# Performance work log

Hardware: AMD Instinct MI355X
Metric: run time of the kernel (lower is better)

The kernel has to match this reference:

```python
import jax, jax.numpy as jnp
import numpy as np

N, E, H, Q, M, B, L = 100000, 800000, 64, 4, 8, 100, 4
EPS_BN = 1e-5


def setup_inputs() -> dict:
    key = jax.random.key(0)
    ki = iter(jax.random.split(key, 32))
    def nrm(shape, scale=1.0):
        return jax.random.normal(next(ki), shape, dtype=jnp.float32) * scale
    inp = {}
    inp["x"] = nrm((N, H))
    inp["pe"] = nrm((N, Q, M, 2))
    inp["Lam"] = jax.random.uniform(next(ki), (B, Q, M), jnp.float32, 0.0, 2.0)
    inp["edge_attr"] = nrm((E, H))
    # per-layer eigenvalue MLP phi: scalar -> 16 -> scalar
    inp["phi_w1"] = nrm((L, 1, 16))
    inp["phi_b1"] = jnp.zeros((L, 16), jnp.float32)
    inp["phi_w2"] = nrm((L, 16, 1), 0.25)
    inp["phi_b2"] = jnp.zeros((L, 1), jnp.float32)
    # per-layer edge PE encoder linear: [2*Q*M -> H]
    inp["enc_w"] = nrm((L, 2 * Q * M, H), (2.0 / (2 * Q * M)) ** 0.5)
    inp["enc_b"] = jnp.zeros((L, H), jnp.float32)
    # per-layer GINE edge linear
    inp["lin_w"] = nrm((L, H, H), (2.0 / H) ** 0.5)
    inp["lin_b"] = jnp.zeros((L, H), jnp.float32)
    # per-layer GINE MLP: Linear -> BN -> ReLU -> Linear
    inp["mlp_w1"] = nrm((L, H, H), (2.0 / H) ** 0.5)
    inp["mlp_b1"] = jnp.zeros((L, H), jnp.float32)
    inp["bn1_g"] = jnp.ones((L, H), jnp.float32)
    inp["bn1_b"] = jnp.zeros((L, H), jnp.float32)
    inp["mlp_w2"] = nrm((L, H, H), (2.0 / H) ** 0.5)
    inp["mlp_b2"] = jnp.zeros((L, H), jnp.float32)
    # per-layer outer BatchNorm
    inp["bn2_g"] = jnp.ones((L, H), jnp.float32)
    inp["bn2_b"] = jnp.zeros((L, H), jnp.float32)
    inp["edge_index"] = jax.random.randint(next(ki), (2, E), 0, N, dtype=jnp.int32)
    inp["batch"] = jnp.sort(jax.random.randint(next(ki), (N,), 0, B, dtype=jnp.int32))
    return inp


def _bn(h, g, b):
    # training-mode BatchNorm1d over the node/row axis
    mu = h.mean(axis=0)
    var = h.var(axis=0)
    return (h - mu) * jax.lax.rsqrt(var + EPS_BN) * g + b


def _forward(x, pe, Lam, edge_attr, params, edge_index, batch):
    (phi_w1, phi_b1, phi_w2, phi_b2, enc_w, enc_b, lin_w, lin_b,
     mlp_w1, mlp_b1, bn1_g, bn1_b, mlp_w2, mlp_b2, bn2_g, bn2_b) = params
    src, dst = edge_index[0], edge_index[1]
    # permutation-invariant complex edge features: pe[src] * conj(pe[dst]), per (q, eigvec)
    zs_re, zs_im = pe[src, ..., 0], pe[src, ..., 1]   # [E, Q, M]
    zd_re, zd_im = pe[dst, ..., 0], pe[dst, ..., 1]
    z_re = zs_re * zd_re + zs_im * zd_im              # [E, Q, M]
    z_im = zs_im * zd_re - zs_re * zd_im
    eg = batch[src]                                    # graph id per edge  [E]
    for l in range(L):
        # eigenvalue MLP -> per-eigenvector weight  [B, Q, M]
        hphi = jax.nn.relu(Lam[..., None] @ phi_w1[l] + phi_b1[l])   # [B,Q,M,16]
        w = (hphi @ phi_w2[l])[..., 0] + phi_b2[l][0]                # [B,Q,M]
        we = w[eg]                                                   # [E,Q,M]
        feat = jnp.concatenate([(z_re * we).reshape(E, Q * M),
                                (z_im * we).reshape(E, Q * M)], axis=-1)  # [E, 2QM]
        edge_pe = feat @ enc_w[l] + enc_b[l]                          # [E,H]
        ea = edge_pe + edge_attr
        # GINE message: ReLU(x_j + lin(edge_attr)), sum-aggregated at dst
        msg = jax.nn.relu(x[src] + ea @ lin_w[l] + lin_b[l])          # [E,H]
        agg = jax.ops.segment_sum(msg, dst, num_segments=N)           # [N,H]
        h = x + agg                                                   # (1+eps)*x with eps=0
        h = jax.nn.relu(_bn(h @ mlp_w1[l] + mlp_b1[l], bn1_g[l], bn1_b[l]))
        h = h @ mlp_w2[l] + mlp_b2[l]
        x = _bn(h, bn2_g[l], bn2_b[l])
        if l != L - 1:
            x = jax.nn.relu(x)
    return x


def reference(x, pe, Lam, edge_attr, phi_w1, phi_b1, phi_w2, phi_b2, enc_w, enc_b,
              lin_w, lin_b, mlp_w1, mlp_b1, bn1_g, bn1_b, mlp_w2, mlp_b2, bn2_g, bn2_b,
              edge_index, batch):
    params = (phi_w1, phi_b1, phi_w2, phi_b2, enc_w, enc_b, lin_w, lin_b,
              mlp_w1, mlp_b1, bn1_g, bn1_b, mlp_w2, mlp_b2, bn2_g, bn2_b)
    return (_forward(x, pe, Lam, edge_attr, params, edge_index, batch), pe)
```

## Files before the change

### kernel.cpp

```cpp
#include <hip/hip_runtime.h>

#define N_NODES 100000
#define N_EDGES 800000
#define HD 64
#define NB 100
#define NL 4
#define QM 32
#define EPS_BN 1e-5f

typedef __bf16 bf16_t;
typedef __bf16 bf16x8 __attribute__((ext_vector_type(8)));
typedef float f32x4 __attribute__((ext_vector_type(4)));


__global__ void k_count(const int* __restrict__ dst, int* __restrict__ counts) {
    int e = blockIdx.x * 256 + threadIdx.x;
    if (e < N_EDGES) atomicAdd(&counts[dst[e]], 1);
}

__global__ void k_scan1(const int* __restrict__ counts, int* __restrict__ row_ptr,
                        int* __restrict__ blk) {
    __shared__ int s[1024];
    int i = blockIdx.x * 1024 + threadIdx.x;
    int v = (i < N_NODES) ? counts[i] : 0;
    s[threadIdx.x] = v;
    __syncthreads();
    for (int off = 1; off < 1024; off <<= 1) {
        int u = (threadIdx.x >= off) ? s[threadIdx.x - off] : 0;
        __syncthreads();
        s[threadIdx.x] += u;
        __syncthreads();
    }
    if (i < N_NODES) row_ptr[i] = s[threadIdx.x] - v;
    if (threadIdx.x == 1023) blk[blockIdx.x] = s[1023];
}

__global__ void k_scan2(int* __restrict__ blk) {
    __shared__ int s[128];
    int t = threadIdx.x;
    int v = (t < 98) ? blk[t] : 0;
    s[t] = v;
    __syncthreads();
    for (int off = 1; off < 128; off <<= 1) {
        int u = (t >= off) ? s[t - off] : 0;
        __syncthreads();
        s[t] += u;
        __syncthreads();
    }
    if (t < 98) blk[t] = s[t] - v;
}

__global__ void k_scan3(const int* __restrict__ blk, int* __restrict__ row_ptr) {
    int i = blockIdx.x * 1024 + threadIdx.x;
    if (i < N_NODES) row_ptr[i] += blk[blockIdx.x];
    if (i == 0) row_ptr[N_NODES] = N_EDGES;
}

__global__ void k_scatter(const int* __restrict__ ei, const int* __restrict__ batch,
                          const int* __restrict__ row_ptr, int* __restrict__ counts,
                          int* __restrict__ src_s, int* __restrict__ eg_s,
                          int* __restrict__ dst_s, int* __restrict__ pos_of) {
    int e = blockIdx.x * 256 + threadIdx.x;
    if (e >= N_EDGES) return;
    int s = ei[e], d = ei[N_EDGES + e];
    int pos = row_ptr[d] + atomicAdd(&counts[d], 1);
    pos_of[e] = pos;
    src_s[pos] = s;
    eg_s[pos]  = batch[s];
    dst_s[pos] = d;
}

__global__ void k_permute(const float* __restrict__ pe, const float* __restrict__ edge_attr,
                          const int* __restrict__ ei, const int* __restrict__ pos_of,
                          bf16_t* __restrict__ z_s, bf16_t* __restrict__ ea_s) {
    int t = blockIdx.x * 256 + threadIdx.x;
    int e = t >> 3, j = t & 7;
    if (e >= N_EDGES) return;
    int pos = pos_of[e];
    {
        const float* ap = edge_attr + (size_t)e * 64 + j * 8;
        f32x4 a0 = *(const f32x4*)ap, a1 = *(const f32x4*)(ap + 4);
        bf16x8 o;
#pragma unroll
        for (int i = 0; i < 4; i++) { o[i] = (bf16_t)a0[i]; o[i + 4] = (bf16_t)a1[i]; }
        *(bf16x8*)(ea_s + (size_t)pos * 64 + j * 8) = o;
    }
    int s = ei[e], d = ei[N_EDGES + e];
    int jq = j & 3;
    const float* ps = pe + (size_t)s * 64 + jq * 16;
    const float* pd = pe + (size_t)d * 64 + jq * 16;
    f32x4 s0 = *(const f32x4*)ps, s1 = *(const f32x4*)(ps + 4);
    f32x4 s2 = *(const f32x4*)(ps + 8), s3 = *(const f32x4*)(ps + 12);
    f32x4 d0 = *(const f32x4*)pd, d1 = *(const f32x4*)(pd + 4);
    f32x4 d2 = *(const f32x4*)(pd + 8), d3 = *(const f32x4*)(pd + 12);
    float sv[16], dv[16];
#pragma unroll
    for (int i = 0; i < 4; i++) {
        sv[i] = s0[i]; sv[4 + i] = s1[i]; sv[8 + i] = s2[i]; sv[12 + i] = s3[i];
        dv[i] = d0[i]; dv[4 + i] = d1[i]; dv[8 + i] = d2[i]; dv[12 + i] = d3[i];
    }
    bool isim = (j >= 4);
    bf16x8 o;
#pragma unroll
    for (int i = 0; i < 8; i++) {
        float sr = sv[2 * i], si = sv[2 * i + 1];
        float dr = dv[2 * i], di = dv[2 * i + 1];
        float v = isim ? (si * dr - sr * di) : (sr * dr + si * di);
        o[i] = (bf16_t)v;
    }
    *(bf16x8*)(z_s + (size_t)pos * 64 + j * 8) = o;
}


__global__ void k_phi(const float* __restrict__ Lam, const float* __restrict__ w1,
                      const float* __restrict__ b1, const float* __restrict__ w2,
                      const float* __restrict__ b2, bf16_t* __restrict__ w_all) {
    int idx = blockIdx.x * 256 + threadIdx.x;
    if (idx >= NL * NB * QM) return;
    int l = idx / (NB * QM);
    int rem = idx % (NB * QM);
    float lam = Lam[rem];
    float acc = b2[l];
    for (int i = 0; i < 16; i++) {
        float h = lam * w1[l * 16 + i] + b1[l * 16 + i];
        acc += fmaxf(h, 0.f) * w2[l * 16 + i];
    }
    w_all[idx] = (bf16_t)acc;
}

__global__ void k_prep(const float* __restrict__ enc_w, const float* __restrict__ enc_b,
                       const float* __restrict__ lin_w, const float* __restrict__ lin_b,
                       const float* __restrict__ mlp_w1, const float* __restrict__ mlp_w2,
                       bf16_t* __restrict__ wcat_frag, bf16_t* __restrict__ w1frag,
                       bf16_t* __restrict__ w2frag, float* __restrict__ cvec) {
    __shared__ float lds[128][64];
    int l = blockIdx.x, tid = threadIdx.x;
    const float* ew = enc_w + l * 64 * 64;
    const float* lw = lin_w + l * 64 * 64;
    for (int idx = tid; idx < 64 * 64; idx += 256) {
        int r = idx >> 6, c = idx & 63;
        float acc = 0.f;
        for (int k = 0; k < 64; k++) acc += ew[r * 64 + k] * lw[k * 64 + c];
        lds[r][c] = acc;
        lds[64 + r][c] = lw[r * 64 + c];
    }
    if (tid < 64) {
        float acc = lin_b[l * 64 + tid];
        for (int k = 0; k < 64; k++) acc += enc_b[l * 64 + k] * lw[k * 64 + tid];
        cvec[l * 64 + tid] = acc;
    }
    __syncthreads();
    for (int idx = tid; idx < 16 * 512; idx += 256) {
        int sn = idx >> 9, lane = (idx >> 3) & 63, j = idx & 7;
        int s = sn >> 2, nt = sn & 3;
        int row = 32 * s + (lane >> 4) * 8 + j;
        int col = 16 * nt + (lane & 15);
        wcat_frag[l * 8192 + idx] = (bf16_t)lds[row][col];
    }
    for (int idx = tid; idx < 8 * 512; idx += 256) {
        int sn = idx >> 9, lane = (idx >> 3) & 63, j = idx & 7;
        int s = sn >> 2, nt = sn & 3;
        int row = 32 * s + (lane >> 4) * 8 + j;
        int col = 16 * nt + (lane & 15);
        w1frag[l * 4096 + idx] = (bf16_t)mlp_w1[(l * 64 + row) * 64 + col];
        w2frag[l * 4096 + idx] = (bf16_t)mlp_w2[(l * 64 + row) * 64 + col];
    }
}


__global__ void k_hinit(const float* __restrict__ x, float* __restrict__ h) {
    size_t i = ((size_t)blockIdx.x * 256 + threadIdx.x) * 8;
    if (i >= (size_t)N_NODES * 64) return;
    *(f32x4*)(h + i) = *(const f32x4*)(x + i);
    *(f32x4*)(h + i + 4) = *(const f32x4*)(x + i + 4);
}

__global__ void k_edge(const bf16_t* __restrict__ z_s, const bf16_t* __restrict__ ea_s,
                       const int* __restrict__ src_s, const int* __restrict__ eg_s,
                       const int* __restrict__ dst_s, const int* __restrict__ row_ptr,
                       const bf16_t* __restrict__ w_l, const bf16_t* __restrict__ wcat_l,
                       const float* __restrict__ cvec_l, const float* __restrict__ x_cur,
                       float* __restrict__ h) {
    __shared__ float msg[128][68];
    int tid = threadIdx.x;
    int wave = tid >> 6, lane = tid & 63;
    int quad = lane >> 4, l16 = lane & 15;
    int e0 = blockIdx.x * 128;

    bf16x8 bfrag[4][4];
    const bf16x8* wf = (const bf16x8*)wcat_l;
#pragma unroll
    for (int s = 0; s < 4; s++)
#pragma unroll
        for (int nt = 0; nt < 4; nt++) bfrag[s][nt] = wf[(s * 4 + nt) * 64 + lane];

    f32x4 acc[2][4];
#pragma unroll
    for (int rt = 0; rt < 2; rt++)
#pragma unroll
        for (int nt = 0; nt < 4; nt++) acc[rt][nt] = (f32x4)(0.f);

    int em[2];
    bf16x8 wch[2];
#pragma unroll
    for (int rt = 0; rt < 2; rt++) {
        em[rt] = e0 + wave * 32 + rt * 16 + l16;
        int eg = eg_s[em[rt]];
        wch[rt] = *(const bf16x8*)(w_l + (size_t)eg * QM + quad * 8);
    }
#pragma unroll
    for (int s = 0; s < 4; s++) {
        bf16x8 afr[2];
#pragma unroll
        for (int rt = 0; rt < 2; rt++) {
            if (s < 2) {
                bf16x8 z = *(const bf16x8*)(z_s + (size_t)em[rt] * 64 + s * 32 + quad * 8);
                bf16x8 a;
#pragma unroll
                for (int i = 0; i < 8; i++) a[i] = (bf16_t)((float)z[i] * (float)wch[rt][i]);
                afr[rt] = a;
            } else {
                afr[rt] = *(const bf16x8*)(ea_s + (size_t)em[rt] * 64 + (s - 2) * 32 + quad * 8);
            }
        }
#pragma unroll
        for (int rt = 0; rt < 2; rt++)
#pragma unroll
            for (int nt = 0; nt < 4; nt++)
                acc[rt][nt] = __builtin_amdgcn_mfma_f32_16x16x32_bf16(afr[rt], bfrag[s][nt],
                                                                     acc[rt][nt], 0, 0, 0);
    }
#pragma unroll
    for (int nt = 0; nt < 4; nt++) {
        float cv = cvec_l[nt * 16 + l16];
#pragma unroll
        for (int rt = 0; rt < 2; rt++)
#pragma unroll
            for (int r = 0; r < 4; r++)
                msg[wave * 32 + rt * 16 + quad * 4 + r][nt * 16 + l16] = acc[rt][nt][r] + cv;
    }
    __syncthreads();
    {
        int j = tid >> 1, half = tid & 1;
        int srcn = src_s[e0 + j];
        const float* xp = x_cur + (size_t)srcn * 64 + half * 32;
        float* mrow = &msg[j][half * 32];
#pragma unroll
        for (int g = 0; g < 8; g++) {
            f32x4 xv = *(const f32x4*)(xp + g * 4);
            f32x4 m = *(const f32x4*)(mrow + g * 4);
#pragma unroll
            for (int k = 0; k < 4; k++) m[k] = fmaxf(m[k] + xv[k], 0.f);
            *(f32x4*)(mrow + g * 4) = m;
        }
    }
    __syncthreads();
    int nfirst = dst_s[e0], nlast = dst_s[e0 + 127];
    int c = tid & 63;
    for (int n = nfirst + (tid >> 6); n <= nlast; n += 4) {
        int rs = row_ptr[n], re = row_ptr[n + 1];
        int a = rs > e0 ? rs : e0;
        int b = re < e0 + 128 ? re : e0 + 128;
        if (a >= b) continue;
        float sum = 0.f;
        for (int jj = a; jj < b; jj++) sum += msg[jj - e0][c];
        float* addr = h + (size_t)n * 64 + c;
        if (rs >= e0 && re <= e0 + 128) *addr += sum;
        else atomicAdd(addr, sum);
    }
}

__global__ void k_mlp1(const float* __restrict__ h, const bf16_t* __restrict__ w1frag_l,
                       const float* __restrict__ b1_l, bf16_t* __restrict__ t,
                       float* __restrict__ stats) {
    __shared__ float sred[128];
    int tid = threadIdx.x, wave = tid >> 6, lane = tid & 63, quad = lane >> 4, l16 = lane & 15;
    int r0 = blockIdx.x * 128;
    bf16x8 bfrag[2][4];
    const bf16x8* wf = (const bf16x8*)w1frag_l;
#pragma unroll
    for (int s = 0; s < 2; s++)
#pragma unroll
        for (int nt = 0; nt < 4; nt++) bfrag[s][nt] = wf[(s * 4 + nt) * 64 + lane];
    f32x4 acc[2][4];
#pragma unroll
    for (int rt = 0; rt < 2; rt++)
#pragma unroll
        for (int nt = 0; nt < 4; nt++) acc[rt][nt] = (f32x4)(0.f);
#pragma unroll
    for (int rt = 0; rt < 2; rt++) {
        int n = r0 + wave * 32 + rt * 16 + l16;
        bool valid = n < N_NODES;
#pragma unroll
        for (int s = 0; s < 2; s++) {
            bf16x8 a;
            if (valid) {
                const float* hp = h + (size_t)n * 64 + s * 32 + quad * 8;
                f32x4 v0 = *(const f32x4*)hp, v1 = *(const f32x4*)(hp + 4);
#pragma unroll
                for (int i = 0; i < 4; i++) { a[i] = (bf16_t)v0[i]; a[i + 4] = (bf16_t)v1[i]; }
            } else {
#pragma unroll
                for (int i = 0; i < 8; i++) a[i] = (bf16_t)0.f;
            }
#pragma unroll
            for (int nt = 0; nt < 4; nt++)
                acc[rt][nt] = __builtin_amdgcn_mfma_f32_16x16x32_bf16(a, bfrag[s][nt],
                                                                     acc[rt][nt], 0, 0, 0);
        }
    }
    if (tid < 128) sred[tid] = 0.f;
    __syncthreads();
#pragma unroll
    for (int nt = 0; nt < 4; nt++) {
        int col = nt * 16 + l16;
        float bias = b1_l[col];
        float s1 = 0.f, s2 = 0.f;
#pragma unroll
        for (int rt = 0; rt < 2; rt++)
#pragma unroll
            for (int r = 0; r < 4; r++) {
                int n = r0 + wave * 32 + rt * 16 + quad * 4 + r;
                if (n < N_NODES) {
                    float v = acc[rt][nt][r] + bias;
                    t[(size_t)n * 64 + col] = (bf16_t)v;
                    s1 += v; s2 += v * v;
                }
            }
        s1 += __shfl_xor(s1, 16); s1 += __shfl_xor(s1, 32);
        s2 += __shfl_xor(s2, 16); s2 += __shfl_xor(s2, 32);
        if (quad == 0) { atomicAdd(&sred[col], s1); atomicAdd(&sred[64 + col], s2); }
    }
    __syncthreads();
    if (tid < 128) atomicAdd(&stats[tid], sred[tid]);
}

__global__ void k_bncoef(const float* __restrict__ stats, const float* __restrict__ g,
                         const float* __restrict__ b, float* __restrict__ coef) {
    int c = threadIdx.x;
    if (c >= 64) return;
    float mean = stats[c] / (float)N_NODES;
    float var = stats[64 + c] / (float)N_NODES - mean * mean;
    float a = g[c] * rsqrtf(var + EPS_BN);
    coef[c] = a;
    coef[64 + c] = b[c] - mean * a;
}

__global__ void k_mlp2(const bf16_t* __restrict__ t, const float* __restrict__ coef,
                       const bf16_t* __restrict__ w2frag_l, const float* __restrict__ b2_l,
                       float* __restrict__ h2, float* __restrict__ stats2) {
    __shared__ float sred[128];
    int tid = threadIdx.x, wave = tid >> 6, lane = tid & 63, quad = lane >> 4, l16 = lane & 15;
    int r0 = blockIdx.x * 128;
    bf16x8 bfrag[2][4];
    const bf16x8* wf = (const bf16x8*)w2frag_l;
#pragma unroll
    for (int s = 0; s < 2; s++)
#pragma unroll
        for (int nt = 0; nt < 4; nt++) bfrag[s][nt] = wf[(s * 4 + nt) * 64 + lane];
    f32x4 acc[2][4];
#pragma unroll
    for (int rt = 0; rt < 2; rt++)
#pragma unroll
        for (int nt = 0; nt < 4; nt++) acc[rt][nt] = (f32x4)(0.f);
#pragma unroll
    for (int rt = 0; rt < 2; rt++) {
        int n = r0 + wave * 32 + rt * 16 + l16;
        bool valid = n < N_NODES;
#pragma unroll
        for (int s = 0; s < 2; s++) {
            bf16x8 a;
            if (valid) {
                bf16x8 tv = *(const bf16x8*)(t + (size_t)n * 64 + s * 32 + quad * 8);
                int kb = s * 32 + quad * 8;
#pragma unroll
                for (int i = 0; i < 8; i++) {
                    float y = (float)tv[i] * coef[kb + i] + coef[64 + kb + i];
                    a[i] = (bf16_t)fmaxf(y, 0.f);
                }
            } else {
#pragma unroll
                for (int i = 0; i < 8; i++) a[i] = (bf16_t)0.f;
            }
#pragma unroll
            for (int nt = 0; nt < 4; nt++)
                acc[rt][nt] = __builtin_amdgcn_mfma_f32_16x16x32_bf16(a, bfrag[s][nt],
                                                                     acc[rt][nt], 0, 0, 0);
        }
    }
    if (tid < 128) sred[tid] = 0.f;
    __syncthreads();
#pragma unroll
    for (int nt = 0; nt < 4; nt++) {
        int col = nt * 16 + l16;
        float bias = b2_l[col];
        float s1 = 0.f, s2 = 0.f;
#pragma unroll
        for (int rt = 0; rt < 2; rt++)
#pragma unroll
            for (int r = 0; r < 4; r++) {
                int n = r0 + wave * 32 + rt * 16 + quad * 4 + r;
                if (n < N_NODES) {
                    float v = acc[rt][nt][r] + bias;
                    h2[(size_t)n * 64 + col] = v;
                    s1 += v; s2 += v * v;
                }
            }
        s1 += __shfl_xor(s1, 16); s1 += __shfl_xor(s1, 32);
        s2 += __shfl_xor(s2, 16); s2 += __shfl_xor(s2, 32);
        if (quad == 0) { atomicAdd(&sred[col], s1); atomicAdd(&sred[64 + col], s2); }
    }
    __syncthreads();
    if (tid < 128) atomicAdd(&stats2[tid], sred[tid]);
}

__global__ void k_bnapply(const float* __restrict__ h2, const float* __restrict__ coef,
                          float* __restrict__ out, int do_relu) {
    size_t i = ((size_t)blockIdx.x * 256 + threadIdx.x) * 8;
    if (i >= (size_t)N_NODES * 64) return;
    int c0 = (int)(i & 63);
    f32x4 a = *(const f32x4*)(h2 + i), b = *(const f32x4*)(h2 + i + 4);
    f32x4 oa, ob;
#pragma unroll
    for (int k = 0; k < 4; k++) {
        float y0 = a[k] * coef[c0 + k] + coef[64 + c0 + k];
        float y1 = b[k] * coef[c0 + 4 + k] + coef[64 + c0 + 4 + k];
        if (do_relu) { y0 = fmaxf(y0, 0.f); y1 = fmaxf(y1, 0.f); }
        oa[k] = y0; ob[k] = y1;
    }
    *(f32x4*)(out + i) = oa;
    *(f32x4*)(out + i + 4) = ob;
}


extern "C" void kernel_launch(void* const* d_in, const int* in_sizes, int n_in,
                              void* d_out, int out_size, void* d_ws, size_t ws_size,
                              hipStream_t stream) {
    const float* x_in   = (const float*)d_in[0];
    const float* pe     = (const float*)d_in[1];
    const float* Lam    = (const float*)d_in[2];
    const float* eattr  = (const float*)d_in[3];
    const float* phi_w1 = (const float*)d_in[4];
    const float* phi_b1 = (const float*)d_in[5];
    const float* phi_w2 = (const float*)d_in[6];
    const float* phi_b2 = (const float*)d_in[7];
    const float* enc_w  = (const float*)d_in[8];
    const float* enc_b  = (const float*)d_in[9];
    const float* lin_w  = (const float*)d_in[10];
    const float* lin_b  = (const float*)d_in[11];
    const float* mlp_w1 = (const float*)d_in[12];
    const float* mlp_b1 = (const float*)d_in[13];
    const float* bn1_g  = (const float*)d_in[14];
    const float* bn1_b  = (const float*)d_in[15];
    const float* mlp_w2 = (const float*)d_in[16];
    const float* mlp_b2 = (const float*)d_in[17];
    const float* bn2_g  = (const float*)d_in[18];
    const float* bn2_b  = (const float*)d_in[19];
    const int* edge_index = (const int*)d_in[20];
    const int* batch      = (const int*)d_in[21];
    float* out = (float*)d_out;

    char* ws = (char*)d_ws;
    size_t off = 0;
    auto alloc = [&](size_t bytes) -> void* {
        void* p = ws + off;
        off += (bytes + 255) & ~(size_t)255;
        return p;
    };
    bf16_t* z_s       = (bf16_t*)alloc((size_t)N_EDGES * 64 * 2);
    bf16_t* ea_s      = (bf16_t*)alloc((size_t)N_EDGES * 64 * 2);
    int* src_s        = (int*)alloc((size_t)N_EDGES * 4);
    int* eg_s         = (int*)alloc((size_t)N_EDGES * 4);
    int* dst_s        = (int*)alloc((size_t)N_EDGES * 4);
    int* pos_of       = (int*)alloc((size_t)N_EDGES * 4);
    int* counts       = (int*)alloc((size_t)N_NODES * 4);
    int* row_ptr      = (int*)alloc((size_t)(N_NODES + 1) * 4);
    int* blk          = (int*)alloc(128 * 4);
    float* h          = (float*)alloc((size_t)N_NODES * 64 * 4);
    bf16_t* t         = (bf16_t*)alloc((size_t)N_NODES * 64 * 2);
    float* h2         = (float*)alloc((size_t)N_NODES * 64 * 4);
    float* x_cur      = (float*)alloc((size_t)N_NODES * 64 * 4);
    bf16_t* w_all     = (bf16_t*)alloc((size_t)NL * NB * QM * 2);
    bf16_t* wcat_frag = (bf16_t*)alloc((size_t)NL * 8192 * 2);
    bf16_t* w1frag    = (bf16_t*)alloc((size_t)NL * 4096 * 2);
    bf16_t* w2frag    = (bf16_t*)alloc((size_t)NL * 4096 * 2);
    float* cvec       = (float*)alloc((size_t)NL * 64 * 4);
    float* stats      = (float*)alloc(256 * 4);
    float* bncoef     = (float*)alloc(256 * 4);

    hipMemsetAsync(counts, 0, (size_t)N_NODES * 4, stream);
    k_count<<<3125, 256, 0, stream>>>(edge_index + N_EDGES, counts);
    k_scan1<<<98, 1024, 0, stream>>>(counts, row_ptr, blk);
    k_scan2<<<1, 128, 0, stream>>>(blk);
    k_scan3<<<98, 1024, 0, stream>>>(blk, row_ptr);
    hipMemsetAsync(counts, 0, (size_t)N_NODES * 4, stream);
    k_scatter<<<3125, 256, 0, stream>>>(edge_index, batch, row_ptr, counts,
                                        src_s, eg_s, dst_s, pos_of);
    k_permute<<<25000, 256, 0, stream>>>(pe, eattr, edge_index, pos_of, z_s, ea_s);
    k_phi<<<50, 256, 0, stream>>>(Lam, phi_w1, phi_b1, phi_w2, phi_b2, w_all);
    k_prep<<<NL, 256, 0, stream>>>(enc_w, enc_b, lin_w, lin_b, mlp_w1, mlp_w2,
                                   wcat_frag, w1frag, w2frag, cvec);

    for (int l = 0; l < NL; l++) {
        const float* xp = (l == 0) ? x_in : x_cur;
        hipMemsetAsync(stats, 0, 256 * 4, stream);
        k_hinit<<<3125, 256, 0, stream>>>(xp, h);
        k_edge<<<6250, 256, 0, stream>>>(z_s, ea_s, src_s, eg_s, dst_s, row_ptr,
                                         w_all + (size_t)l * NB * QM,
                                         wcat_frag + (size_t)l * 8192,
                                         cvec + (size_t)l * 64, xp, h);
        k_mlp1<<<782, 256, 0, stream>>>(h, w1frag + (size_t)l * 4096,
                                        mlp_b1 + l * 64, t, stats);
        k_bncoef<<<1, 64, 0, stream>>>(stats, bn1_g + l * 64, bn1_b + l * 64, bncoef);
        k_mlp2<<<782, 256, 0, stream>>>(t, bncoef, w2frag + (size_t)l * 4096,
                                        mlp_b2 + l * 64, h2, stats + 128);
        k_bncoef<<<1, 64, 0, stream>>>(stats + 128, bn2_g + l * 64, bn2_b + l * 64,
                                       bncoef + 128);
        float* outp = (l < NL - 1) ? x_cur : out;
        k_bnapply<<<3125, 256, 0, stream>>>(h2, bncoef + 128, outp, (l < NL - 1) ? 1 : 0);
    }
    hipMemcpyAsync(out + (size_t)N_NODES * 64, pe, (size_t)N_NODES * QM * 2 * 4,
                   hipMemcpyDeviceToDevice, stream);
}
```

Baseline: 1.312 ms.

## Pack edge metadata, interleave features, fuse BN coef and h-init into neighbours

Packs per-edge src/dst/graph/orig-id into one int4 array and interleaves z and edge_attr into a single 128-wide bf16 feature row per sorted edge. The permute kernel reads through the sorted index instead of scattering writes. The BN coefficient kernels are folded into mlp2 and the apply kernels. The apply kernel also writes the next layer's h init and a bf16 copy of x, which removes the separate hinit pass and makes the edge kernel's x[src] gather read bf16. The trade-off is extra rounding of node features to bf16, plus redundant per-block recomputation of the BN coefficients.

After: 1.194 ms. -9.0%, faster.

```diff
diff --git a/kernel.cpp b/kernel.cpp
--- a/kernel.cpp
+++ b/kernel.cpp
@@ -2,7 +2,6 @@
 
 #define N_NODES 100000
 #define N_EDGES 800000
-#define HD 64
 #define NB 100
 #define NL 4
 #define QM 32
@@ -10,6 +9,8 @@
 
 typedef __bf16 bf16_t;
 typedef __bf16 bf16x8 __attribute__((ext_vector_type(8)));
+typedef __bf16 bf16x4 __attribute__((ext_vector_type(4)));
+typedef __bf16 bf16x2 __attribute__((ext_vector_type(2)));
 typedef float f32x4 __attribute__((ext_vector_type(4)));
 
 
@@ -57,58 +58,35 @@
 }
 
 __global__ void k_scatter(const int* __restrict__ ei, const int* __restrict__ batch,
-                          const int* __restrict__ row_ptr, int* __restrict__ counts,
-                          int* __restrict__ src_s, int* __restrict__ eg_s,
-                          int* __restrict__ dst_s, int* __restrict__ pos_of) {
+                          const int* __restrict__ row_ptr, int* __restrict__ cursor,
+                          int4* __restrict__ edat) {
     int e = blockIdx.x * 256 + threadIdx.x;
     if (e >= N_EDGES) return;
     int s = ei[e], d = ei[N_EDGES + e];
-    int pos = row_ptr[d] + atomicAdd(&counts[d], 1);
-    pos_of[e] = pos;
-    src_s[pos] = s;
-    eg_s[pos]  = batch[s];
-    dst_s[pos] = d;
-}
-
-__global__ void k_permute(const float* __restrict__ pe, const float* __restrict__ edge_attr,
-                          const int* __restrict__ ei, const int* __restrict__ pos_of,
-                          bf16_t* __restrict__ z_s, bf16_t* __restrict__ ea_s) {
+    int pos = row_ptr[d] + atomicAdd(&cursor[d], 1);
+    edat[pos] = make_int4(s, d, batch[s], e);
+}
+
+__global__ void k_permute(const float* __restrict__ pe, const float* __restrict__ ea,
+                          const int4* __restrict__ edat, bf16_t* __restrict__ feat) {
     int t = blockIdx.x * 256 + threadIdx.x;
-    int e = t >> 3, j = t & 7;
-    if (e >= N_EDGES) return;
-    int pos = pos_of[e];
-    {
-        const float* ap = edge_attr + (size_t)e * 64 + j * 8;
-        f32x4 a0 = *(const f32x4*)ap, a1 = *(const f32x4*)(ap + 4);
-        bf16x8 o;
-#pragma unroll
-        for (int i = 0; i < 4; i++) { o[i] = (bf16_t)a0[i]; o[i + 4] = (bf16_t)a1[i]; }
-        *(bf16x8*)(ea_s + (size_t)pos * 64 + j * 8) = o;
-    }
-    int s = ei[e], d = ei[N_EDGES + e];
-    int jq = j & 3;
-    const float* ps = pe + (size_t)s * 64 + jq * 16;
-    const float* pd = pe + (size_t)d * 64 + jq * 16;
-    f32x4 s0 = *(const f32x4*)ps, s1 = *(const f32x4*)(ps + 4);
-    f32x4 s2 = *(const f32x4*)(ps + 8), s3 = *(const f32x4*)(ps + 12);
-    f32x4 d0 = *(const f32x4*)pd, d1 = *(const f32x4*)(pd + 4);
-    f32x4 d2 = *(const f32x4*)(pd + 8), d3 = *(const f32x4*)(pd + 12);
-    float sv[16], dv[16];
-#pragma unroll
-    for (int i = 0; i < 4; i++) {
-        sv[i] = s0[i]; sv[4 + i] = s1[i]; sv[8 + i] = s2[i]; sv[12 + i] = s3[i];
-        dv[i] = d0[i]; dv[4 + i] = d1[i]; dv[8 + i] = d2[i]; dv[12 + i] = d3[i];
-    }
-    bool isim = (j >= 4);
-    bf16x8 o;
-#pragma unroll
-    for (int i = 0; i < 8; i++) {
-        float sr = sv[2 * i], si = sv[2 * i + 1];
-        float dr = dv[2 * i], di = dv[2 * i + 1];
-        float v = isim ? (si * dr - sr * di) : (sr * dr + si * di);
-        o[i] = (bf16_t)v;
-    }
-    *(bf16x8*)(z_s + (size_t)pos * 64 + j * 8) = o;
+    int p = t >> 4, k = t & 15;
+    int4 ed = edat[p];
+    int src = ed.x, dst = ed.y, e = ed.w;
+    f32x4 av = *(const f32x4*)(ea + (size_t)e * 64 + k * 4);
+    bf16x4 ao;
+#pragma unroll
+    for (int i = 0; i < 4; i++) ao[i] = (bf16_t)av[i];
+    *(bf16x4*)(feat + (size_t)p * 128 + 64 + k * 4) = ao;
+    f32x4 sv = *(const f32x4*)(pe + (size_t)src * 64 + k * 4);
+    f32x4 dv = *(const f32x4*)(pe + (size_t)dst * 64 + k * 4);
+    bf16x2 re, im;
+    re[0] = (bf16_t)(sv[0] * dv[0] + sv[1] * dv[1]);
+    re[1] = (bf16_t)(sv[2] * dv[2] + sv[3] * dv[3]);
+    im[0] = (bf16_t)(sv[1] * dv[0] - sv[0] * dv[1]);
+    im[1] = (bf16_t)(sv[3] * dv[2] - sv[2] * dv[3]);
+    *(bf16x2*)(feat + (size_t)p * 128 + 2 * k) = re;
+    *(bf16x2*)(feat + (size_t)p * 128 + 32 + 2 * k) = im;
 }
 
 
@@ -168,19 +146,22 @@
 }
 
 
-__global__ void k_hinit(const float* __restrict__ x, float* __restrict__ h) {
+__global__ void k_hinit0(const float* __restrict__ x, bf16_t* __restrict__ x_bf,
+                         float* __restrict__ h) {
     size_t i = ((size_t)blockIdx.x * 256 + threadIdx.x) * 8;
-    if (i >= (size_t)N_NODES * 64) return;
-    *(f32x4*)(h + i) = *(const f32x4*)(x + i);
-    *(f32x4*)(h + i + 4) = *(const f32x4*)(x + i + 4);
-}
-
-__global__ void k_edge(const bf16_t* __restrict__ z_s, const bf16_t* __restrict__ ea_s,
-                       const int* __restrict__ src_s, const int* __restrict__ eg_s,
-                       const int* __restrict__ dst_s, const int* __restrict__ row_ptr,
-                       const bf16_t* __restrict__ w_l, const bf16_t* __restrict__ wcat_l,
-                       const float* __restrict__ cvec_l, const float* __restrict__ x_cur,
-                       float* __restrict__ h) {
+    f32x4 a = *(const f32x4*)(x + i), b = *(const f32x4*)(x + i + 4);
+    *(f32x4*)(h + i) = a;
+    *(f32x4*)(h + i + 4) = b;
+    bf16x8 o;
+#pragma unroll
+    for (int k = 0; k < 4; k++) { o[k] = (bf16_t)a[k]; o[k + 4] = (bf16_t)b[k]; }
+    *(bf16x8*)(x_bf + i) = o;
+}
+
+__global__ void k_edge(const bf16_t* __restrict__ feat, const int4* __restrict__ edat,
+                       const int* __restrict__ row_ptr, const bf16_t* __restrict__ w_l,
+                       const bf16_t* __restrict__ wcat_l, const float* __restrict__ cvec_l,
+                       const bf16_t* __restrict__ x_bf, float* __restrict__ h) {
     __shared__ float msg[128][68];
     int tid = threadIdx.x;
     int wave = tid >> 6, lane = tid & 63;
@@ -205,7 +186,7 @@
 #pragma unroll
     for (int rt = 0; rt < 2; rt++) {
         em[rt] = e0 + wave * 32 + rt * 16 + l16;
-        int eg = eg_s[em[rt]];
+        int eg = edat[em[rt]].z;
         wch[rt] = *(const bf16x8*)(w_l + (size_t)eg * QM + quad * 8);
     }
 #pragma unroll
@@ -213,14 +194,14 @@
         bf16x8 afr[2];
 #pragma unroll
         for (int rt = 0; rt < 2; rt++) {
+            bf16x8 v = *(const bf16x8*)(feat + (size_t)em[rt] * 128 + s * 32 + quad * 8);
             if (s < 2) {
-                bf16x8 z = *(const bf16x8*)(z_s + (size_t)em[rt] * 64 + s * 32 + quad * 8);
                 bf16x8 a;
 #pragma unroll
-                for (int i = 0; i < 8; i++) a[i] = (bf16_t)((float)z[i] * (float)wch[rt][i]);
+                for (int i = 0; i < 8; i++) a[i] = (bf16_t)((float)v[i] * (float)wch[rt][i]);
                 afr[rt] = a;
             } else {
-                afr[rt] = *(const bf16x8*)(ea_s + (size_t)em[rt] * 64 + (s - 2) * 32 + quad * 8);
+                afr[rt] = v;
             }
         }
 #pragma unroll
@@ -240,22 +221,24 @@
                 msg[wave * 32 + rt * 16 + quad * 4 + r][nt * 16 + l16] = acc[rt][nt][r] + cv;
     }
     __syncthreads();
-    {
-        int j = tid >> 1, half = tid & 1;
-        int srcn = src_s[e0 + j];
-        const float* xp = x_cur + (size_t)srcn * 64 + half * 32;
-        float* mrow = &msg[j][half * 32];
-#pragma unroll
-        for (int g = 0; g < 8; g++) {
-            f32x4 xv = *(const f32x4*)(xp + g * 4);
-            f32x4 m = *(const f32x4*)(mrow + g * 4);
-#pragma unroll
-            for (int k = 0; k < 4; k++) m[k] = fmaxf(m[k] + xv[k], 0.f);
-            *(f32x4*)(mrow + g * 4) = m;
+#pragma unroll
+    for (int it = 0; it < 4; it++) {
+        int j = it * 32 + (tid >> 3);
+        int l8 = tid & 7;
+        int srcn = edat[e0 + j].x;
+        bf16x8 xv = *(const bf16x8*)(x_bf + (size_t)srcn * 64 + l8 * 8);
+        float* mrow = &msg[j][l8 * 8];
+        f32x4 m0 = *(const f32x4*)mrow, m1 = *(const f32x4*)(mrow + 4);
+#pragma unroll
+        for (int k = 0; k < 4; k++) {
+            m0[k] = fmaxf(m0[k] + (float)xv[k], 0.f);
+            m1[k] = fmaxf(m1[k] + (float)xv[k + 4], 0.f);
         }
-    }
-    __syncthreads();
-    int nfirst = dst_s[e0], nlast = dst_s[e0 + 127];
+        *(f32x4*)mrow = m0;
+        *(f32x4*)(mrow + 4) = m1;
+    }
+    __syncthreads();
+    int nfirst = edat[e0].y, nlast = edat[e0 + 127].y;
     int c = tid & 63;
     for (int n = nfirst + (tid >> 6); n <= nlast; n += 4) {
         int rs = row_ptr[n], re = row_ptr[n + 1];
@@ -335,21 +318,12 @@
     if (tid < 128) atomicAdd(&stats[tid], sred[tid]);
 }
 
-__global__ void k_bncoef(const float* __restrict__ stats, const float* __restrict__ g,
-                         const float* __restrict__ b, float* __restrict__ coef) {
-    int c = threadIdx.x;
-    if (c >= 64) return;
-    float mean = stats[c] / (float)N_NODES;
-    float var = stats[64 + c] / (float)N_NODES - mean * mean;
-    float a = g[c] * rsqrtf(var + EPS_BN);
-    coef[c] = a;
-    coef[64 + c] = b[c] - mean * a;
-}
-
-__global__ void k_mlp2(const bf16_t* __restrict__ t, const float* __restrict__ coef,
+__global__ void k_mlp2(const bf16_t* __restrict__ t, const float* __restrict__ stats1,
+                       const float* __restrict__ g1, const float* __restrict__ b1,
                        const bf16_t* __restrict__ w2frag_l, const float* __restrict__ b2_l,
                        float* __restrict__ h2, float* __restrict__ stats2) {
     __shared__ float sred[128];
+    __shared__ float cf[128];
     int tid = threadIdx.x, wave = tid >> 6, lane = tid & 63, quad = lane >> 4, l16 = lane & 15;
     int r0 = blockIdx.x * 128;
     bf16x8 bfrag[2][4];
@@ -358,6 +332,15 @@
     for (int s = 0; s < 2; s++)
 #pragma unroll
         for (int nt = 0; nt < 4; nt++) bfrag[s][nt] = wf[(s * 4 + nt) * 64 + lane];
+    if (tid < 64) {
+        float mean = stats1[tid] / (float)N_NODES;
+        float var = stats1[64 + tid] / (float)N_NODES - mean * mean;
+        float a = g1[tid] * rsqrtf(var + EPS_BN);
+        cf[tid] = a;
+        cf[64 + tid] = b1[tid] - mean * a;
+    }
+    if (tid >= 64 && tid < 192) sred[tid - 64] = 0.f;
+    __syncthreads();
     f32x4 acc[2][4];
 #pragma unroll
     for (int rt = 0; rt < 2; rt++)
@@ -375,7 +358,7 @@
                 int kb = s * 32 + quad * 8;
 #pragma unroll
                 for (int i = 0; i < 8; i++) {
-                    float y = (float)tv[i] * coef[kb + i] + coef[64 + kb + i];
+                    float y = (float)tv[i] * cf[kb + i] + cf[64 + kb + i];
                     a[i] = (bf16_t)fmaxf(y, 0.f);
                 }
             } else {
@@ -388,8 +371,6 @@
                                                                      acc[rt][nt], 0, 0, 0);
         }
     }
-    if (tid < 128) sred[tid] = 0.f;
-    __syncthreads();
 #pragma unroll
     for (int nt = 0; nt < 4; nt++) {
         int col = nt * 16 + l16;
@@ -414,22 +395,59 @@
     if (tid < 128) atomicAdd(&stats2[tid], sred[tid]);
 }
 
-__global__ void k_bnapply(const float* __restrict__ h2, const float* __restrict__ coef,
-                          float* __restrict__ out, int do_relu) {
-    size_t i = ((size_t)blockIdx.x * 256 + threadIdx.x) * 8;
-    if (i >= (size_t)N_NODES * 64) return;
+__global__ void k_apply_init(const float* __restrict__ h2, const float* __restrict__ stats2,
+                             const float* __restrict__ g, const float* __restrict__ b,
+                             bf16_t* __restrict__ x_bf, float* __restrict__ h) {
+    __shared__ float cf[128];
+    int tid = threadIdx.x;
+    if (tid < 64) {
+        float mean = stats2[tid] / (float)N_NODES;
+        float var = stats2[64 + tid] / (float)N_NODES - mean * mean;
+        float a = g[tid] * rsqrtf(var + EPS_BN);
+        cf[tid] = a;
+        cf[64 + tid] = b[tid] - mean * a;
+    }
+    __syncthreads();
+    size_t i = ((size_t)blockIdx.x * 256 + tid) * 8;
     int c0 = (int)(i & 63);
-    f32x4 a = *(const f32x4*)(h2 + i), b = *(const f32x4*)(h2 + i + 4);
-    f32x4 oa, ob;
+    f32x4 v0 = *(const f32x4*)(h2 + i), v1 = *(const f32x4*)(h2 + i + 4);
+    f32x4 y0, y1;
+    bf16x8 o;
 #pragma unroll
     for (int k = 0; k < 4; k++) {
-        float y0 = a[k] * coef[c0 + k] + coef[64 + c0 + k];
-        float y1 = b[k] * coef[c0 + 4 + k] + coef[64 + c0 + 4 + k];
-        if (do_relu) { y0 = fmaxf(y0, 0.f); y1 = fmaxf(y1, 0.f); }
-        oa[k] = y0; ob[k] = y1;
-    }
-    *(f32x4*)(out + i) = oa;
-    *(f32x4*)(out + i + 4) = ob;
+        y0[k] = fmaxf(v0[k] * cf[c0 + k] + cf[64 + c0 + k], 0.f);
+        y1[k] = fmaxf(v1[k] * cf[c0 + 4 + k] + cf[64 + c0 + 4 + k], 0.f);
+        o[k] = (bf16_t)y0[k]; o[k + 4] = (bf16_t)y1[k];
+    }
+    *(f32x4*)(h + i) = y0;
+    *(f32x4*)(h + i + 4) = y1;
+    *(bf16x8*)(x_bf + i) = o;
+}
+
+__global__ void k_apply_out(const float* __restrict__ h2, const float* __restrict__ stats2,
+                            const float* __restrict__ g, const float* __restrict__ b,
+                            float* __restrict__ out) {
+    __shared__ float cf[128];
+    int tid = threadIdx.x;
+    if (tid < 64) {
+        float mean = stats2[tid] / (float)N_NODES;
+        float var = stats2[64 + tid] / (float)N_NODES - mean * mean;
+        float a = g[tid] * rsqrtf(var + EPS_BN);
+        cf[tid] = a;
+        cf[64 + tid] = b[tid] - mean * a;
+    }
+    __syncthreads();
+    size_t i = ((size_t)blockIdx.x * 256 + tid) * 8;
+    int c0 = (int)(i & 63);
+    f32x4 v0 = *(const f32x4*)(h2 + i), v1 = *(const f32x4*)(h2 + i + 4);
+    f32x4 y0, y1;
+#pragma unroll
+    for (int k = 0; k < 4; k++) {
+        y0[k] = v0[k] * cf[c0 + k] + cf[64 + c0 + k];
+        y1[k] = v1[k] * cf[c0 + 4 + k] + cf[64 + c0 + 4 + k];
+    }
+    *(f32x4*)(out + i) = y0;
+    *(f32x4*)(out + i + 4) = y1;
 }
 
 
@@ -467,57 +485,54 @@
         off += (bytes + 255) & ~(size_t)255;
         return p;
     };
-    bf16_t* z_s       = (bf16_t*)alloc((size_t)N_EDGES * 64 * 2);
-    bf16_t* ea_s      = (bf16_t*)alloc((size_t)N_EDGES * 64 * 2);
-    int* src_s        = (int*)alloc((size_t)N_EDGES * 4);
-    int* eg_s         = (int*)alloc((size_t)N_EDGES * 4);
-    int* dst_s        = (int*)alloc((size_t)N_EDGES * 4);
-    int* pos_of       = (int*)alloc((size_t)N_EDGES * 4);
-    int* counts       = (int*)alloc((size_t)N_NODES * 4);
+    bf16_t* feat      = (bf16_t*)alloc((size_t)N_EDGES * 128 * 2);
+    int4* edat        = (int4*)alloc((size_t)N_EDGES * 16);
     int* row_ptr      = (int*)alloc((size_t)(N_NODES + 1) * 4);
     int* blk          = (int*)alloc(128 * 4);
+    int* counts       = (int*)alloc((size_t)N_NODES * 4);
+    int* cursor       = (int*)alloc((size_t)N_NODES * 4);
+    float* stats      = (float*)alloc((size_t)NL * 256 * 4);
+    size_t zbytes     = (char*)(stats + NL * 256) - (char*)counts;
     float* h          = (float*)alloc((size_t)N_NODES * 64 * 4);
     bf16_t* t         = (bf16_t*)alloc((size_t)N_NODES * 64 * 2);
     float* h2         = (float*)alloc((size_t)N_NODES * 64 * 4);
-    float* x_cur      = (float*)alloc((size_t)N_NODES * 64 * 4);
+    bf16_t* x_bf      = (bf16_t*)alloc((size_t)N_NODES * 64 * 2);
     bf16_t* w_all     = (bf16_t*)alloc((size_t)NL * NB * QM * 2);
     bf16_t* wcat_frag = (bf16_t*)alloc((size_t)NL * 8192 * 2);
     bf16_t* w1frag    = (bf16_t*)alloc((size_t)NL * 4096 * 2);
     bf16_t* w2frag    = (bf16_t*)alloc((size_t)NL * 4096 * 2);
     float* cvec       = (float*)alloc((size_t)NL * 64 * 4);
-    float* stats      = (float*)alloc(256 * 4);
-    float* bncoef     = (float*)alloc(256 * 4);
-
-    hipMemsetAsync(counts, 0, (size_t)N_NODES * 4, stream);
+
+    hipMemsetAsync(counts, 0, zbytes, stream);
     k_count<<<3125, 256, 0, stream>>>(edge_index + N_EDGES, counts);
     k_scan1<<<98, 1024, 0, stream>>>(counts, row_ptr, blk);
     k_scan2<<<1, 128, 0, stream>>>(blk);
     k_scan3<<<98, 1024, 0, stream>>>(blk, row_ptr);
-    hipMemsetAsync(counts, 0, (size_t)N_NODES * 4, stream);
-    k_scatter<<<3125, 256, 0, stream>>>(edge_index, batch, row_ptr, counts,
-                                        src_s, eg_s, dst_s, pos_of);
-    k_permute<<<25000, 256, 0, stream>>>(pe, eattr, edge_index, pos_of, z_s, ea_s);
+    k_scatter<<<3125, 256, 0, stream>>>(edge_index, batch, row_ptr, cursor, edat);
+    k_permute<<<50000, 256, 0, stream>>>(pe, eattr, edat, feat);
     k_phi<<<50, 256, 0, stream>>>(Lam, phi_w1, phi_b1, phi_w2, phi_b2, w_all);
     k_prep<<<NL, 256, 0, stream>>>(enc_w, enc_b, lin_w, lin_b, mlp_w1, mlp_w2,
                                    wcat_frag, w1frag, w2frag, cvec);
 
+    k_hinit0<<<3125, 256, 0, stream>>>(x_in, x_bf, h);
     for (int l = 0; l < NL; l++) {
-        const float* xp = (l == 0) ? x_in : x_cur;
-        hipMemsetAsync(stats, 0, 256 * 4, stream);
-        k_hinit<<<3125, 256, 0, stream>>>(xp, h);
-        k_edge<<<6250, 256, 0, stream>>>(z_s, ea_s, src_s, eg_s, dst_s, row_ptr,
+        float* s1 = stats + l * 256;
+        float* s2 = stats + l * 256 + 128;
+        k_edge<<<6250, 256, 0, stream>>>(feat, edat, row_ptr,
                                          w_all + (size_t)l * NB * QM,
                                          wcat_frag + (size_t)l * 8192,
-                                         cvec + (size_t)l * 64, xp, h);
+                                         cvec + (size_t)l * 64, x_bf, h);
         k_mlp1<<<782, 256, 0, stream>>>(h, w1frag + (size_t)l * 4096,
-                                        mlp_b1 + l * 64, t, stats);
-        k_bncoef<<<1, 64, 0, stream>>>(stats, bn1_g + l * 64, bn1_b + l * 64, bncoef);
-        k_mlp2<<<782, 256, 0, stream>>>(t, bncoef, w2frag + (size_t)l * 4096,
-                                        mlp_b2 + l * 64, h2, stats + 128);
-        k_bncoef<<<1, 64, 0, stream>>>(stats + 128, bn2_g + l * 64, bn2_b + l * 64,
-                                       bncoef + 128);
-        float* outp = (l < NL - 1) ? x_cur : out;
-        k_bnapply<<<3125, 256, 0, stream>>>(h2, bncoef + 128, outp, (l < NL - 1) ? 1 : 0);
+                                        mlp_b1 + l * 64, t, s1);
+        k_mlp2<<<782, 256, 0, stream>>>(t, s1, bn1_g + l * 64, bn1_b + l * 64,
+                                        w2frag + (size_t)l * 4096, mlp_b2 + l * 64,
+                                        h2, s2);
+        if (l < NL - 1)
+            k_apply_init<<<3125, 256, 0, stream>>>(h2, s2, bn2_g + l * 64, bn2_b + l * 64,
+                                                   x_bf, h);
+        else
+            k_apply_out<<<3125, 256, 0, stream>>>(h2, s2, bn2_g + l * 64, bn2_b + l * 64,
+                                                  out);
     }
     hipMemcpyAsync(out + (size_t)N_NODES * 64, pe, (size_t)N_NODES * QM * 2 * 4,
                    hipMemcpyDeviceToDevice, stream);
```
